# Optimization experiments

Hardware: AMD Instinct MI355X
Metric: run time of the kernel (lower is better)

Reference implementation:

```python
import jax, jax.numpy as jnp
import numpy as np

B, L, H, HKV, D, HID, FFN = 32, 4096, 32, 2, 128, 4096, 13696
ROT = 64  # rotary_dim = kv_channels // 2 (GLM style)
EPS = 1e-5


def setup_inputs() -> dict:
    key = jax.random.key(0)
    ks = jax.random.split(key, 9)
    s = 0.02
    return {
        "hidden_states": jax.random.normal(ks[0], (B, HID), jnp.float32),
        "context_lens": jax.random.randint(ks[1], (B,), 1, L - 1, dtype=jnp.int32),
        "key_cache": jax.random.normal(ks[2], (B, L, HKV, D), jnp.float32),
        "value_cache": jax.random.normal(ks[3], (B, L, HKV, D), jnp.float32),
        "w_ln1": jnp.ones((HID,), jnp.float32),
        "w_ln2": jnp.ones((HID,), jnp.float32),
        "w_qkv": jax.random.normal(ks[4], (HID, H * D + 2 * HKV * D), jnp.float32) * s,
        "b_qkv": jax.random.normal(ks[5], (H * D + 2 * HKV * D,), jnp.float32) * s,
        "w_dense": jax.random.normal(ks[6], (H * D, HID), jnp.float32) * s,
        "w_h4h": jax.random.normal(ks[7], (HID, 2 * FFN), jnp.float32) * s,
        "w_4hh": jax.random.normal(ks[8], (FFN, HID), jnp.float32) * s,
    }


def rmsnorm(x, w):
    v = jnp.mean(x.astype(jnp.float32) ** 2, axis=-1, keepdims=True)
    return (w * (x * jax.lax.rsqrt(v + EPS))).astype(x.dtype)


def apply_rope(x, pos):
    # x: [B, heads, D]; GPT-J interleaved rotary on first ROT dims (glm=True)
    half = ROT // 2
    inv = 1.0 / (10000.0 ** (jnp.arange(half, dtype=jnp.float32) / half))
    f = pos.astype(jnp.float32)[:, None] * inv[None, :]          # [B, half]
    cos, sin = jnp.cos(f)[:, None, :], jnp.sin(f)[:, None, :]    # [B,1,half]
    xr, xp = x[..., :ROT], x[..., ROT:]
    x1, x2 = xr[..., 0::2], xr[..., 1::2]
    rot = jnp.stack([x1 * cos - x2 * sin, x2 * cos + x1 * sin], axis=-1).reshape(xr.shape)
    return jnp.concatenate([rot, xp], axis=-1)


def reference(hidden_states, context_lens, key_cache, value_cache,
              w_ln1, w_ln2, w_qkv, b_qkv, w_dense, w_h4h, w_4hh):
    # input RMSNorm
    ln1 = rmsnorm(hidden_states, w_ln1)
    # fused QKV projection (add_qkv_bias=True)
    qkv = ln1 @ w_qkv + b_qkv
    q, k, v = jnp.split(qkv, [H * D, H * D + HKV * D], axis=-1)
    q = apply_rope(q.reshape(B, H, D), context_lens)
    k = apply_rope(k.reshape(B, HKV, D), context_lens)
    v = v.reshape(B, HKV, D)
    # write new K/V into the paged cache at this token's slot
    kc = key_cache.at[jnp.arange(B), context_lens].set(k)
    vc = value_cache.at[jnp.arange(B), context_lens].set(v)
    # GQA attention: 32 q heads grouped over 2 kv heads
    qg = q.reshape(B, HKV, H // HKV, D)
    scores = jnp.einsum('bghd,blgd->bghl', qg, kc) * (D ** -0.5)
    mask = jnp.arange(L)[None, :] <= context_lens[:, None]       # [B, L]
    scores = jnp.where(mask[:, None, None, :], scores, -jnp.inf)
    p = jax.nn.softmax(scores, axis=-1)
    ctx = jnp.einsum('bghl,blgd->bghd', p, vc).reshape(B, H * D)
    attn_out = ctx @ w_dense                                     # add_bias_linear=False
    x = hidden_states + attn_out                                  # residual pre-LN
    ln2 = rmsnorm(x, w_ln2)
    g, u = jnp.split(ln2 @ w_h4h, 2, axis=-1)
    out = (jax.nn.silu(g) * u) @ w_4hh + x
    return out
```

## Files before the change

kernel.cpp:

```cpp
#include <hip/hip_runtime.h>
#include <hip/hip_bf16.h>

#define B_    32
#define L_    4096
#define H_    32
#define HKV_  2
#define GQ_   16
#define D_    128
#define HID_  4096
#define FFN_  13696
#define NQKV_ 4608
#define ROT_  64
#define EPS_  1e-5f

#define WAVE_POS_ 128
#define NSPLIT_   32

typedef __attribute__((ext_vector_type(8))) __bf16 bf16x8;
typedef __attribute__((ext_vector_type(4))) float  f32x4;

__global__ __launch_bounds__(1024) void rmsnorm1_k(const float* __restrict__ x,
                                                   const float* __restrict__ w,
                                                   __bf16* __restrict__ out)
{
    int b = blockIdx.x;
    const float* row = x + (size_t)b * HID_;
    float vals[4];
    float ss = 0.f;
#pragma unroll
    for (int i = 0; i < 4; ++i) {
        vals[i] = row[threadIdx.x + i * 1024];
        ss += vals[i] * vals[i];
    }
#pragma unroll
    for (int m = 1; m < 64; m <<= 1) ss += __shfl_xor(ss, m);
    __shared__ float wred[16];
    if ((threadIdx.x & 63) == 0) wred[threadIdx.x >> 6] = ss;
    __syncthreads();
    ss = 0.f;
#pragma unroll
    for (int wv = 0; wv < 16; ++wv) ss += wred[wv];
    float rs = rsqrtf(ss / HID_ + EPS_);
#pragma unroll
    for (int i = 0; i < 4; ++i) {
        int idx = threadIdx.x + i * 1024;
        out[(size_t)b * HID_ + idx] = (__bf16)(w[idx] * vals[i] * rs);
    }
}

template<int K, int N, int KSPLIT>
__global__ __launch_bounds__(256) void gemm16(const __bf16* __restrict__ A,
                                              const float* __restrict__ W,
                                              float* __restrict__ Cp)
{
    static_assert(K % 32 == 0, "K");
    constexpr int ksteps = K / 32;
    constexpr int nch    = KSPLIT * 4;
    const int lane = threadIdx.x & 63;
    const int wid  = threadIdx.x >> 6;
    const int n0   = blockIdx.x * 32;
    const int r    = lane & 15;
    const int g4   = lane >> 4;
    const int cid  = blockIdx.y * 4 + wid;
    const int s0   = (ksteps * cid) / nch;
    const int s1   = (ksteps * (cid + 1)) / nch;
    const int kk_b = lane >> 3;
    const int c4   = (lane & 7) * 4;

    __shared__ __bf16 tiles[4][32][40];
    __bf16 (*tile)[40] = tiles[wid];

    f32x4 acc00 = {0.f,0.f,0.f,0.f}, acc01 = acc00, acc10 = acc00, acc11 = acc00;
    const __bf16* a0p = A + (size_t)r * K;
    const __bf16* a1p = A + (size_t)(r + 16) * K;

    float4 pf[4];
    auto issue = [&](int s) {
        const float* wk = W + (size_t)(s * 32 + kk_b) * N + n0 + c4;
#pragma unroll
        for (int it = 0; it < 4; ++it)
            pf[it] = *(const float4*)(wk + (size_t)(it * 8) * N);
    };

    if (s0 < s1) issue(s0);
    for (int s = s0; s < s1; ++s) {
        float4 cur[4];
#pragma unroll
        for (int it = 0; it < 4; ++it) cur[it] = pf[it];
        if (s + 1 < s1) issue(s + 1);
#pragma unroll
        for (int it = 0; it < 4; ++it) {
            int kk = it * 8 + kk_b;
            tile[c4 + 0][kk] = (__bf16)cur[it].x;
            tile[c4 + 1][kk] = (__bf16)cur[it].y;
            tile[c4 + 2][kk] = (__bf16)cur[it].z;
            tile[c4 + 3][kk] = (__bf16)cur[it].w;
        }
        asm volatile("s_waitcnt lgkmcnt(0)" ::: "memory");
        __builtin_amdgcn_sched_barrier(0);
        bf16x8 b0  = *(const bf16x8*)&tile[r][g4 * 8];
        bf16x8 b1  = *(const bf16x8*)&tile[r + 16][g4 * 8];
        bf16x8 av0 = *(const bf16x8*)(a0p + s * 32 + g4 * 8);
        bf16x8 av1 = *(const bf16x8*)(a1p + s * 32 + g4 * 8);
        acc00 = __builtin_amdgcn_mfma_f32_16x16x32_bf16(av0, b0, acc00, 0, 0, 0);
        acc10 = __builtin_amdgcn_mfma_f32_16x16x32_bf16(av1, b0, acc10, 0, 0, 0);
        acc01 = __builtin_amdgcn_mfma_f32_16x16x32_bf16(av0, b1, acc01, 0, 0, 0);
        acc11 = __builtin_amdgcn_mfma_f32_16x16x32_bf16(av1, b1, acc11, 0, 0, 0);
        asm volatile("s_waitcnt lgkmcnt(0)" ::: "memory");
        __builtin_amdgcn_sched_barrier(0);
    }

    __shared__ float red[4][32][32];
#pragma unroll
    for (int i = 0; i < 4; ++i) {
        red[wid][g4 * 4 + i][r]           = acc00[i];
        red[wid][g4 * 4 + i][16 + r]      = acc01[i];
        red[wid][16 + g4 * 4 + i][r]      = acc10[i];
        red[wid][16 + g4 * 4 + i][16 + r] = acc11[i];
    }
    __syncthreads();
    for (int idx = threadIdx.x; idx < 1024; idx += 256) {
        int row = idx >> 5, col = idx & 31;
        float v = red[0][row][col] + red[1][row][col] + red[2][row][col] + red[3][row][col];
        Cp[((size_t)blockIdx.y * 32 + row) * N + n0 + col] = v;
    }
}

__global__ __launch_bounds__(1024) void qkv_epi_k(const float* __restrict__ part,
                                                  const float* __restrict__ bias,
                                                  const int* __restrict__ ctxl,
                                                  __bf16* __restrict__ qbf,
                                                  float* __restrict__ knew,
                                                  float* __restrict__ vnew)
{
    __shared__ float rowv[NQKV_];
    __shared__ float cs[32], sn[32];
    int b = blockIdx.x;
    int pos = ctxl[b];
    if (threadIdx.x < 32) {
        int t = threadIdx.x;
        float inv = powf(10000.f, -(float)t * (1.0f / 32.0f));
        float f = (float)pos * inv;
        float sv, cv; sincosf(f, &sv, &cv);
        cs[t] = cv; sn[t] = sv;
    }
    for (int i = threadIdx.x; i < NQKV_; i += 1024) {
        float v = bias[i];
#pragma unroll
        for (int p = 0; p < 4; ++p) v += part[((size_t)p * B_ + b) * NQKV_ + i];
        rowv[i] = v;
    }
    __syncthreads();
    const float qscale = 0.08838834764831845f;
    for (int i = threadIdx.x; i < HID_; i += 1024) {
        int d = i & 127;
        float o;
        if (d < ROT_) {
            int t = d >> 1;
            float cv = cs[t], sv = sn[t];
            float x1 = rowv[i & ~1], x2 = rowv[i | 1];
            o = (d & 1) ? (x2 * cv + x1 * sv) : (x1 * cv - x2 * sv);
        } else o = rowv[i];
        qbf[(size_t)b * HID_ + i] = (__bf16)(o * qscale);
    }
    if (threadIdx.x < HKV_ * D_) {
        int i = threadIdx.x;
        int d = i & 127;
        float o;
        if (d < ROT_) {
            int t = d >> 1;
            float cv = cs[t], sv = sn[t];
            float x1 = rowv[HID_ + (i & ~1)], x2 = rowv[HID_ + (i | 1)];
            o = (d & 1) ? (x2 * cv + x1 * sv) : (x1 * cv - x2 * sv);
        } else o = rowv[HID_ + i];
        knew[(size_t)b * HKV_ * D_ + i] = o;
        vnew[(size_t)b * HKV_ * D_ + i] = rowv[HID_ + HKV_ * D_ + i];
    }
}

__global__ __launch_bounds__(256) void attn_k(const float* __restrict__ kc,
                                              const float* __restrict__ vc,
                                              const float* __restrict__ knew,
                                              const float* __restrict__ vnew,
                                              const __bf16* __restrict__ qbf,
                                              const int* __restrict__ ctxl,
                                              float* __restrict__ part)
{
    const int bg  = blockIdx.x;
    const int b   = bg >> 1, g = bg & 1;
    const int wid = threadIdx.x >> 6;
    const int split = blockIdx.y * 4 + wid;
    const int ctx = ctxl[b];
    const int p0  = split * WAVE_POS_;
    __shared__ __bf16 plds_all[4][16][40];
    if (p0 > ctx) return;
    const int pend = min(p0 + WAVE_POS_ - 1, ctx);
    const int lane = threadIdx.x & 63;
    const int r = lane & 15, g4 = lane >> 4;

    bf16x8 qf[4];
    {
        const __bf16* qp = qbf + (size_t)b * HID_ + (g * GQ_ + r) * D_ + g4 * 8;
#pragma unroll
        for (int kk = 0; kk < 4; ++kk) qf[kk] = *(const bf16x8*)(qp + kk * 32);
    }
    f32x4 acc[8];
#pragma unroll
    for (int dt = 0; dt < 8; ++dt) acc[dt] = (f32x4){0.f,0.f,0.f,0.f};
    float m_run[4], l_run[4];
#pragma unroll
    for (int i = 0; i < 4; ++i) { m_run[i] = -1e30f; l_run[i] = 0.f; }

    auto plds = plds_all[wid];
    const float* kbase = kc + ((size_t)b * L_ * HKV_ + g) * D_;
    const float* vbase = vc + ((size_t)b * L_ * HKV_ + g) * D_;
    const float* knp = knew + (size_t)(b * HKV_ + g) * D_;
    const float* vnp = vnew + (size_t)(b * HKV_ + g) * D_;

    for (int pc = p0; pc <= pend; pc += 32) {
        f32x4 sf[2];
#pragma unroll
        for (int pt = 0; pt < 2; ++pt) {
            int pos = pc + pt * 16 + r;
            const float* krow = (pos == ctx) ? knp : kbase + (size_t)pos * (HKV_ * D_);
            f32x4 s = {0.f,0.f,0.f,0.f};
#pragma unroll
            for (int kk = 0; kk < 4; ++kk) {
                const float4* kp = (const float4*)(krow + kk * 32 + g4 * 8);
                float4 fa = kp[0], fb = kp[1];
                bf16x8 kf = { (__bf16)fa.x, (__bf16)fa.y, (__bf16)fa.z, (__bf16)fa.w,
                              (__bf16)fb.x, (__bf16)fb.y, (__bf16)fb.z, (__bf16)fb.w };
                s = __builtin_amdgcn_mfma_f32_16x16x32_bf16(qf[kk], kf, s, 0, 0, 0);
            }
            sf[pt] = s;
        }
#pragma unroll
        for (int pt = 0; pt < 2; ++pt) {
            int pos = pc + pt * 16 + r;
            if (pos > ctx) {
#pragma unroll
                for (int i = 0; i < 4; ++i) sf[pt][i] = -1e30f;
            }
        }
#pragma unroll
        for (int i = 0; i < 4; ++i) {
            float mv = fmaxf(sf[0][i], sf[1][i]);
            mv = fmaxf(mv, __shfl_xor(mv, 1));
            mv = fmaxf(mv, __shfl_xor(mv, 2));
            mv = fmaxf(mv, __shfl_xor(mv, 4));
            mv = fmaxf(mv, __shfl_xor(mv, 8));
            float mnew = fmaxf(m_run[i], mv);
            float sc = __expf(m_run[i] - mnew);
            l_run[i] *= sc;
            m_run[i] = mnew;
#pragma unroll
            for (int dt = 0; dt < 8; ++dt) acc[dt][i] *= sc;
        }
#pragma unroll
        for (int pt = 0; pt < 2; ++pt) {
#pragma unroll
            for (int i = 0; i < 4; ++i) {
                float e = __expf(sf[pt][i] - m_run[i]);
                l_run[i] += e;
                plds[g4 * 4 + i][pt * 16 + r] = (__bf16)e;
            }
        }
        asm volatile("s_waitcnt lgkmcnt(0)" ::: "memory");
        __builtin_amdgcn_sched_barrier(0);
        bf16x8 pa = *(const bf16x8*)&plds[r][g4 * 8];
        const float* vrows[8];
#pragma unroll
        for (int j = 0; j < 8; ++j) {
            int pos = pc + g4 * 8 + j;
            vrows[j] = (pos == ctx) ? vnp : vbase + (size_t)pos * (HKV_ * D_);
        }
#pragma unroll
        for (int dt = 0; dt < 8; ++dt) {
            bf16x8 vf;
#pragma unroll
            for (int j = 0; j < 8; ++j) vf[j] = (__bf16)vrows[j][dt * 16 + r];
            acc[dt] = __builtin_amdgcn_mfma_f32_16x16x32_bf16(pa, vf, acc[dt], 0, 0, 0);
        }
        asm volatile("s_waitcnt lgkmcnt(0)" ::: "memory");
        __builtin_amdgcn_sched_barrier(0);
    }
#pragma unroll
    for (int i = 0; i < 4; ++i) {
        float lv = l_run[i];
        lv += __shfl_xor(lv, 1);
        lv += __shfl_xor(lv, 2);
        lv += __shfl_xor(lv, 4);
        lv += __shfl_xor(lv, 8);
        l_run[i] = lv;
    }
    float* pb = part + ((size_t)bg * NSPLIT_ + split) * 16 * 130;
#pragma unroll
    for (int dt = 0; dt < 8; ++dt)
#pragma unroll
        for (int i = 0; i < 4; ++i)
            pb[(g4 * 4 + i) * 130 + dt * 16 + r] = acc[dt][i];
    if (r == 0) {
#pragma unroll
        for (int i = 0; i < 4; ++i) {
            pb[(g4 * 4 + i) * 130 + 128] = m_run[i];
            pb[(g4 * 4 + i) * 130 + 129] = l_run[i];
        }
    }
}

__global__ __launch_bounds__(1024) void attn_comb_k(const float* __restrict__ part,
                                                    const int* __restrict__ ctxl,
                                                    __bf16* __restrict__ ctxb)
{
    int bg = blockIdx.x;
    int c  = blockIdx.y;
    int b = bg >> 1, g = bg & 1;
    int ctx = ctxl[b];
    int ns = ctx / WAVE_POS_ + 1;
    const float* pb = part + (size_t)bg * NSPLIT_ * 16 * 130;
    __shared__ float mlm[NSPLIT_][16], wgt[NSPLIT_][16];
    __shared__ float Mh[16], Ih[16];
    int t = threadIdx.x;
    if (t < NSPLIT_ * 16) {
        int s = t >> 4, h = t & 15;
        mlm[s][h] = pb[(s * 16 + h) * 130 + 128];
        wgt[s][h] = pb[(s * 16 + h) * 130 + 129];
    }
    __syncthreads();
    if (t < 16) {
        int h = t;
        float M = -1e30f;
        for (int s = 0; s < ns; ++s) M = fmaxf(M, mlm[s][h]);
        float den = 0.f;
        for (int s = 0; s < ns; ++s) den += __expf(mlm[s][h] - M) * wgt[s][h];
        Mh[h] = M; Ih[h] = 1.f / den;
    }
    __syncthreads();
    if (t < NSPLIT_ * 16) {
        int s = t >> 4, h = t & 15;
        wgt[s][h] = __expf(mlm[s][h] - Mh[h]) * Ih[h];
    }
    __syncthreads();
    int h = t >> 6, dd = (t & 63) + c * 64;
    float o = 0.f;
    for (int s = 0; s < ns; ++s)
        o += wgt[s][h] * pb[(s * 16 + h) * 130 + dd];
    ctxb[(size_t)b * HID_ + (g * GQ_ + h) * D_ + dd] = (__bf16)o;
}

__global__ __launch_bounds__(1024) void dense_epi_k(const float* __restrict__ hidden,
                                                    const float* __restrict__ partd,
                                                    const float* __restrict__ wln2,
                                                    float* __restrict__ xout,
                                                    __bf16* __restrict__ a2)
{
    __shared__ float xr[HID_];
    int b = blockIdx.x;
    float ss = 0.f;
    for (int i = threadIdx.x; i < HID_; i += 1024) {
        float v = hidden[(size_t)b * HID_ + i];
#pragma unroll
        for (int p = 0; p < 4; ++p) v += partd[((size_t)p * B_ + b) * HID_ + i];
        xr[i] = v;
        ss += v * v;
        xout[(size_t)b * HID_ + i] = v;
    }
#pragma unroll
    for (int m = 1; m < 64; m <<= 1) ss += __shfl_xor(ss, m);
    __shared__ float wred[16];
    if ((threadIdx.x & 63) == 0) wred[threadIdx.x >> 6] = ss;
    __syncthreads();
    ss = 0.f;
#pragma unroll
    for (int wv = 0; wv < 16; ++wv) ss += wred[wv];
    float rs = rsqrtf(ss / HID_ + EPS_);
    for (int i = threadIdx.x; i < HID_; i += 1024)
        a2[(size_t)b * HID_ + i] = (__bf16)(wln2[i] * xr[i] * rs);
}

__global__ __launch_bounds__(256) void act_k(const float* __restrict__ gu,
                                             __bf16* __restrict__ act)
{
    int i = blockIdx.x * 256 + threadIdx.x;
    int b = blockIdx.y;
    if (i < FFN_) {
        float gv = gu[(size_t)b * 2 * FFN_ + i];
        float uv = gu[(size_t)b * 2 * FFN_ + FFN_ + i];
        float s = gv / (1.f + __expf(-gv));
        act[(size_t)b * FFN_ + i] = (__bf16)(s * uv);
    }
}

__global__ __launch_bounds__(256) void out_epi_k(const float* __restrict__ x,
                                                 const float* __restrict__ part4,
                                                 float* __restrict__ out)
{
    int i = blockIdx.x * 256 + threadIdx.x;
    float v = x[i];
#pragma unroll
    for (int p = 0; p < 4; ++p) v += part4[(size_t)p * (B_ * HID_) + i];
    out[i] = v;
}

extern "C" void kernel_launch(void* const* d_in, const int* in_sizes, int n_in,
                              void* d_out, int out_size, void* d_ws, size_t ws_size,
                              hipStream_t stream)
{
    const float* hidden  = (const float*)d_in[0];
    const int*   ctxl    = (const int*)d_in[1];
    const float* kcache  = (const float*)d_in[2];
    const float* vcache  = (const float*)d_in[3];
    const float* w_ln1   = (const float*)d_in[4];
    const float* w_ln2   = (const float*)d_in[5];
    const float* w_qkv   = (const float*)d_in[6];
    const float* b_qkv   = (const float*)d_in[7];
    const float* w_dense = (const float*)d_in[8];
    const float* w_h4h   = (const float*)d_in[9];
    const float* w_4hh   = (const float*)d_in[10];
    float* out = (float*)d_out;

    char* ws = (char*)d_ws;
    size_t off = 0;
    auto alloc = [&](size_t bytes) -> void* {
        void* p = ws + off;
        off += (bytes + 255) & ~(size_t)255;
        return p;
    };
    __bf16* a0    = (__bf16*)alloc((size_t)B_ * HID_ * 2);
    float*  partq = (float*) alloc((size_t)4 * B_ * NQKV_ * 4);
    __bf16* qbf   = (__bf16*)alloc((size_t)B_ * HID_ * 2);
    float*  knew  = (float*) alloc((size_t)B_ * HKV_ * D_ * 4);
    float*  vnew  = (float*) alloc((size_t)B_ * HKV_ * D_ * 4);
    float*  apart = (float*) alloc((size_t)B_ * HKV_ * NSPLIT_ * 16 * 130 * 4);
    __bf16* ctxb  = (__bf16*)alloc((size_t)B_ * HID_ * 2);
    float*  partd = (float*) alloc((size_t)4 * B_ * HID_ * 4);
    float*  xbuf  = (float*) alloc((size_t)B_ * HID_ * 4);
    __bf16* a2    = (__bf16*)alloc((size_t)B_ * HID_ * 2);
    float*  gu    = (float*) alloc((size_t)B_ * 2 * FFN_ * 4);
    __bf16* actb  = (__bf16*)alloc((size_t)B_ * FFN_ * 2);
    float*  part4 = (float*) alloc((size_t)4 * B_ * HID_ * 4);
    (void)ws_size; (void)in_sizes; (void)n_in; (void)out_size;

    hipLaunchKernelGGL(rmsnorm1_k, dim3(B_), dim3(1024), 0, stream, hidden, w_ln1, a0);
    hipLaunchKernelGGL((gemm16<HID_, NQKV_, 4>), dim3(NQKV_ / 32, 4), dim3(256), 0, stream, a0, w_qkv, partq);
    hipLaunchKernelGGL(qkv_epi_k, dim3(B_), dim3(1024), 0, stream, partq, b_qkv, ctxl, qbf, knew, vnew);
    hipLaunchKernelGGL(attn_k, dim3(B_ * HKV_, NSPLIT_ / 4), dim3(256), 0, stream,
                       kcache, vcache, knew, vnew, qbf, ctxl, apart);
    hipLaunchKernelGGL(attn_comb_k, dim3(B_ * HKV_, 2), dim3(1024), 0, stream, apart, ctxl, ctxb);
    hipLaunchKernelGGL((gemm16<HID_, HID_, 4>), dim3(HID_ / 32, 4), dim3(256), 0, stream, ctxb, w_dense, partd);
    hipLaunchKernelGGL(dense_epi_k, dim3(B_), dim3(1024), 0, stream, hidden, partd, w_ln2, xbuf, a2);
    hipLaunchKernelGGL((gemm16<HID_, 2 * FFN_, 1>), dim3(2 * FFN_ / 32, 1), dim3(256), 0, stream, a2, w_h4h, gu);
    hipLaunchKernelGGL(act_k, dim3((FFN_ + 255) / 256, B_), dim3(256), 0, stream, gu, actb);
    hipLaunchKernelGGL((gemm16<FFN_, HID_, 4>), dim3(HID_ / 32, 4), dim3(256), 0, stream, actb, w_4hh, part4);
    hipLaunchKernelGGL(out_epi_k, dim3(B_ * HID_ / 256), dim3(256), 0, stream, xbuf, part4, out);
}
```

Measured before the change: 290.2 us.

## Stream GEMM weights into a swizzled LDS ring via global_load_lds with wider K-split

The bf16 GEMM is restructured so each block covers 128 output columns, with each wave owning 32 of them across the block's whole K range. This removes the per-block cross-wave LDS reduction. FP32 weight tiles are copied straight from global memory into a 3-deep, XOR-swizzled LDS ring using global_load_lds, with vmcnt waits and barriers for pipelining. The bf16 conversion now happens when the tile is read back from LDS. K-split factors are raised (16 for QKV, dense and 4h→h, 4 for h→4h) to keep enough blocks in flight, and the epilogue kernels now sum the extra partial buffers. This costs more partial-sum traffic and workspace.

```diff
diff --git a/kernel.cpp b/kernel.cpp
--- a/kernel.cpp
+++ b/kernel.cpp
@@ -16,8 +16,18 @@
 #define WAVE_POS_ 128
 #define NSPLIT_   32
 
+#define KS_QKV_  16
+#define KS_DEN_  16
+#define KS_H4H_  4
+#define KS_4HH_  16
+
 typedef __attribute__((ext_vector_type(8))) __bf16 bf16x8;
 typedef __attribute__((ext_vector_type(4))) float  f32x4;
+
+__device__ __forceinline__ void gl_lds16(const float* g, float* l) {
+    __builtin_amdgcn_global_load_lds((const __attribute__((address_space(1))) void*)g,
+                                     (__attribute__((address_space(3))) void*)l, 16, 0, 0);
+}
 
 __global__ __launch_bounds__(1024) void rmsnorm1_k(const float* __restrict__ x,
                                                    const float* __restrict__ w,
@@ -55,74 +65,73 @@
 {
     static_assert(K % 32 == 0, "K");
     constexpr int ksteps = K / 32;
-    constexpr int nch    = KSPLIT * 4;
     const int lane = threadIdx.x & 63;
     const int wid  = threadIdx.x >> 6;
-    const int n0   = blockIdx.x * 32;
+    const int n0   = blockIdx.x * 128;
+    const int cw   = wid * 32;
     const int r    = lane & 15;
     const int g4   = lane >> 4;
-    const int cid  = blockIdx.y * 4 + wid;
-    const int s0   = (ksteps * cid) / nch;
-    const int s1   = (ksteps * (cid + 1)) / nch;
-    const int kk_b = lane >> 3;
-    const int c4   = (lane & 7) * 4;
-
-    __shared__ __bf16 tiles[4][32][40];
-    __bf16 (*tile)[40] = tiles[wid];
+    const int s0   = (ksteps * (int)blockIdx.y) / KSPLIT;
+    const int s1   = (ksteps * (int)(blockIdx.y + 1)) / KSPLIT;
+
+    __shared__ float tiles[3][32][128];
+
+    const int rhalf = lane >> 5;
+    const int mslot = lane & 31;
+    auto stage = [&](int s, float* dst) {
+        if (s >= s1) return;
+#pragma unroll
+        for (int it = 0; it < 4; ++it) {
+            int row  = wid * 8 + it * 2 + rhalf;
+            int gcol = ((((mslot >> 1) ^ (row >> 3)) << 3) | ((mslot & 1) << 2));
+            const float* src = W + (size_t)(s * 32 + row) * N + n0 + gcol;
+            gl_lds16(src, dst + (size_t)(wid * 8 + it * 2) * 128);
+        }
+    };
 
     f32x4 acc00 = {0.f,0.f,0.f,0.f}, acc01 = acc00, acc10 = acc00, acc11 = acc00;
     const __bf16* a0p = A + (size_t)r * K;
     const __bf16* a1p = A + (size_t)(r + 16) * K;
 
-    float4 pf[4];
-    auto issue = [&](int s) {
-        const float* wk = W + (size_t)(s * 32 + kk_b) * N + n0 + c4;
-#pragma unroll
-        for (int it = 0; it < 4; ++it)
-            pf[it] = *(const float4*)(wk + (size_t)(it * 8) * N);
-    };
-
-    if (s0 < s1) issue(s0);
+    stage(s0,     &tiles[0][0][0]);
+    stage(s0 + 1, &tiles[1][0][0]);
+
+    const int c0 = cw + r, c1 = cw + r + 16;
+    const int i0 = (((c0 >> 3) ^ g4) << 3) | (c0 & 7);
+    const int i1 = (((c1 >> 3) ^ g4) << 3) | (c1 & 7);
+
+    int bufc = 0;
     for (int s = s0; s < s1; ++s) {
-        float4 cur[4];
-#pragma unroll
-        for (int it = 0; it < 4; ++it) cur[it] = pf[it];
-        if (s + 1 < s1) issue(s + 1);
-#pragma unroll
-        for (int it = 0; it < 4; ++it) {
-            int kk = it * 8 + kk_b;
-            tile[c4 + 0][kk] = (__bf16)cur[it].x;
-            tile[c4 + 1][kk] = (__bf16)cur[it].y;
-            tile[c4 + 2][kk] = (__bf16)cur[it].z;
-            tile[c4 + 3][kk] = (__bf16)cur[it].w;
-        }
-        asm volatile("s_waitcnt lgkmcnt(0)" ::: "memory");
+        if (s + 1 < s1) asm volatile("s_waitcnt vmcnt(4)" ::: "memory");
+        else            asm volatile("s_waitcnt vmcnt(0)" ::: "memory");
+        __builtin_amdgcn_s_barrier();
         __builtin_amdgcn_sched_barrier(0);
-        bf16x8 b0  = *(const bf16x8*)&tile[r][g4 * 8];
-        bf16x8 b1  = *(const bf16x8*)&tile[r + 16][g4 * 8];
+        int bs = bufc + 2; if (bs >= 3) bs -= 3;
+        stage(s + 2, &tiles[bs][0][0]);
+
         bf16x8 av0 = *(const bf16x8*)(a0p + s * 32 + g4 * 8);
         bf16x8 av1 = *(const bf16x8*)(a1p + s * 32 + g4 * 8);
-        acc00 = __builtin_amdgcn_mfma_f32_16x16x32_bf16(av0, b0, acc00, 0, 0, 0);
-        acc10 = __builtin_amdgcn_mfma_f32_16x16x32_bf16(av1, b0, acc10, 0, 0, 0);
-        acc01 = __builtin_amdgcn_mfma_f32_16x16x32_bf16(av0, b1, acc01, 0, 0, 0);
-        acc11 = __builtin_amdgcn_mfma_f32_16x16x32_bf16(av1, b1, acc11, 0, 0, 0);
-        asm volatile("s_waitcnt lgkmcnt(0)" ::: "memory");
-        __builtin_amdgcn_sched_barrier(0);
-    }
-
-    __shared__ float red[4][32][32];
+        const float (*tile)[128] = tiles[bufc];
+        bf16x8 b0f, b1f;
+#pragma unroll
+        for (int j = 0; j < 8; ++j) {
+            b0f[j] = (__bf16)tile[g4 * 8 + j][i0];
+            b1f[j] = (__bf16)tile[g4 * 8 + j][i1];
+        }
+        acc00 = __builtin_amdgcn_mfma_f32_16x16x32_bf16(av0, b0f, acc00, 0, 0, 0);
+        acc10 = __builtin_amdgcn_mfma_f32_16x16x32_bf16(av1, b0f, acc10, 0, 0, 0);
+        acc01 = __builtin_amdgcn_mfma_f32_16x16x32_bf16(av0, b1f, acc01, 0, 0, 0);
+        acc11 = __builtin_amdgcn_mfma_f32_16x16x32_bf16(av1, b1f, acc11, 0, 0, 0);
+        bufc = (bufc + 1 < 3) ? bufc + 1 : 0;
+    }
+
+    float* cp = Cp + ((size_t)blockIdx.y * 32) * N + n0 + cw;
 #pragma unroll
     for (int i = 0; i < 4; ++i) {
-        red[wid][g4 * 4 + i][r]           = acc00[i];
-        red[wid][g4 * 4 + i][16 + r]      = acc01[i];
-        red[wid][16 + g4 * 4 + i][r]      = acc10[i];
-        red[wid][16 + g4 * 4 + i][16 + r] = acc11[i];
-    }
-    __syncthreads();
-    for (int idx = threadIdx.x; idx < 1024; idx += 256) {
-        int row = idx >> 5, col = idx & 31;
-        float v = red[0][row][col] + red[1][row][col] + red[2][row][col] + red[3][row][col];
-        Cp[((size_t)blockIdx.y * 32 + row) * N + n0 + col] = v;
+        cp[(size_t)(g4 * 4 + i) * N + r]           = acc00[i];
+        cp[(size_t)(g4 * 4 + i) * N + r + 16]      = acc01[i];
+        cp[(size_t)(16 + g4 * 4 + i) * N + r]      = acc10[i];
+        cp[(size_t)(16 + g4 * 4 + i) * N + r + 16] = acc11[i];
     }
 }
 
@@ -147,7 +156,7 @@
     for (int i = threadIdx.x; i < NQKV_; i += 1024) {
         float v = bias[i];
 #pragma unroll
-        for (int p = 0; p < 4; ++p) v += part[((size_t)p * B_ + b) * NQKV_ + i];
+        for (int p = 0; p < KS_QKV_; ++p) v += part[((size_t)p * B_ + b) * NQKV_ + i];
         rowv[i] = v;
     }
     __syncthreads();
@@ -360,7 +369,7 @@
     for (int i = threadIdx.x; i < HID_; i += 1024) {
         float v = hidden[(size_t)b * HID_ + i];
 #pragma unroll
-        for (int p = 0; p < 4; ++p) v += partd[((size_t)p * B_ + b) * HID_ + i];
+        for (int p = 0; p < KS_DEN_; ++p) v += partd[((size_t)p * B_ + b) * HID_ + i];
         xr[i] = v;
         ss += v * v;
         xout[(size_t)b * HID_ + i] = v;
@@ -384,8 +393,13 @@
     int i = blockIdx.x * 256 + threadIdx.x;
     int b = blockIdx.y;
     if (i < FFN_) {
-        float gv = gu[(size_t)b * 2 * FFN_ + i];
-        float uv = gu[(size_t)b * 2 * FFN_ + FFN_ + i];
+        float gv = 0.f, uv = 0.f;
+#pragma unroll
+        for (int p = 0; p < KS_H4H_; ++p) {
+            const float* gp = gu + ((size_t)p * B_ + b) * 2 * FFN_;
+            gv += gp[i];
+            uv += gp[FFN_ + i];
+        }
         float s = gv / (1.f + __expf(-gv));
         act[(size_t)b * FFN_ + i] = (__bf16)(s * uv);
     }
@@ -398,7 +412,7 @@
     int i = blockIdx.x * 256 + threadIdx.x;
     float v = x[i];
 #pragma unroll
-    for (int p = 0; p < 4; ++p) v += part4[(size_t)p * (B_ * HID_) + i];
+    for (int p = 0; p < KS_4HH_; ++p) v += part4[(size_t)p * (B_ * HID_) + i];
     out[i] = v;
 }
 
@@ -427,30 +441,30 @@
         return p;
     };
     __bf16* a0    = (__bf16*)alloc((size_t)B_ * HID_ * 2);
-    float*  partq = (float*) alloc((size_t)4 * B_ * NQKV_ * 4);
+    float*  partq = (float*) alloc((size_t)KS_QKV_ * B_ * NQKV_ * 4);
     __bf16* qbf   = (__bf16*)alloc((size_t)B_ * HID_ * 2);
     float*  knew  = (float*) alloc((size_t)B_ * HKV_ * D_ * 4);
     float*  vnew  = (float*) alloc((size_t)B_ * HKV_ * D_ * 4);
     float*  apart = (float*) alloc((size_t)B_ * HKV_ * NSPLIT_ * 16 * 130 * 4);
     __bf16* ctxb  = (__bf16*)alloc((size_t)B_ * HID_ * 2);
-    float*  partd = (float*) alloc((size_t)4 * B_ * HID_ * 4);
+    float*  partd = (float*) alloc((size_t)KS_DEN_ * B_ * HID_ * 4);
     float*  xbuf  = (float*) alloc((size_t)B_ * HID_ * 4);
     __bf16* a2    = (__bf16*)alloc((size_t)B_ * HID_ * 2);
-    float*  gu    = (float*) alloc((size_t)B_ * 2 * FFN_ * 4);
+    float*  gu    = (float*) alloc((size_t)KS_H4H_ * B_ * 2 * FFN_ * 4);
     __bf16* actb  = (__bf16*)alloc((size_t)B_ * FFN_ * 2);
-    float*  part4 = (float*) alloc((size_t)4 * B_ * HID_ * 4);
+    float*  part4 = (float*) alloc((size_t)KS_4HH_ * B_ * HID_ * 4);
     (void)ws_size; (void)in_sizes; (void)n_in; (void)out_size;
 
     hipLaunchKernelGGL(rmsnorm1_k, dim3(B_), dim3(1024), 0, stream, hidden, w_ln1, a0);
-    hipLaunchKernelGGL((gemm16<HID_, NQKV_, 4>), dim3(NQKV_ / 32, 4), dim3(256), 0, stream, a0, w_qkv, partq);
+    hipLaunchKernelGGL((gemm16<HID_, NQKV_, KS_QKV_>), dim3(NQKV_ / 128, KS_QKV_), dim3(256), 0, stream, a0, w_qkv, partq);
     hipLaunchKernelGGL(qkv_epi_k, dim3(B_), dim3(1024), 0, stream, partq, b_qkv, ctxl, qbf, knew, vnew);
     hipLaunchKernelGGL(attn_k, dim3(B_ * HKV_, NSPLIT_ / 4), dim3(256), 0, stream,
                        kcache, vcache, knew, vnew, qbf, ctxl, apart);
     hipLaunchKernelGGL(attn_comb_k, dim3(B_ * HKV_, 2), dim3(1024), 0, stream, apart, ctxl, ctxb);
-    hipLaunchKernelGGL((gemm16<HID_, HID_, 4>), dim3(HID_ / 32, 4), dim3(256), 0, stream, ctxb, w_dense, partd);
+    hipLaunchKernelGGL((gemm16<HID_, HID_, KS_DEN_>), dim3(HID_ / 128, KS_DEN_), dim3(256), 0, stream, ctxb, w_dense, partd);
     hipLaunchKernelGGL(dense_epi_k, dim3(B_), dim3(1024), 0, stream, hidden, partd, w_ln2, xbuf, a2);
-    hipLaunchKernelGGL((gemm16<HID_, 2 * FFN_, 1>), dim3(2 * FFN_ / 32, 1), dim3(256), 0, stream, a2, w_h4h, gu);
+    hipLaunchKernelGGL((gemm16<HID_, 2 * FFN_, KS_H4H_>), dim3(2 * FFN_ / 128, KS_H4H_), dim3(256), 0, stream, a2, w_h4h, gu);
     hipLaunchKernelGGL(act_k, dim3((FFN_ + 255) / 256, B_), dim3(256), 0, stream, gu, actb);
-    hipLaunchKernelGGL((gemm16<FFN_, HID_, 4>), dim3(HID_ / 32, 4), dim3(256), 0, stream, actb, w_4hh, part4);
+    hipLaunchKernelGGL((gemm16<FFN_, HID_, KS_4HH_>), dim3(HID_ / 128, KS_4HH_), dim3(256), 0, stream, actb, w_4hh, part4);
     hipLaunchKernelGGL(out_epi_k, dim3(B_ * HID_ / 256), dim3(256), 0, stream, xbuf, part4, out);
 }
```

New measurement: 269.0 us. 7.3% less time.
